# Optimization experiments

Measured on AMD Instinct MI355X. Metric: run time of the kernel, lower is better.

Reference implementation:

```python
import jax, jax.numpy as jnp
import numpy as np

PAST = 12
FUTURE = 12
INPUT_SIZE = 256
OUTPUT_SIZE = FUTURE * INPUT_SIZE  # 3072


def setup_inputs() -> dict:
    key = jax.random.key(0)
    k_inp, k_w, k_b = jax.random.split(key, 3)
    inp = jax.random.normal(k_inp, (64, 288, INPUT_SIZE), dtype=jnp.float32)
    fan_in = INPUT_SIZE * PAST
    bound = 1.0 / np.sqrt(fan_in)
    # torch nn.Linear init: U(-1/sqrt(fan_in), 1/sqrt(fan_in)); W is (out, in)
    W = jax.random.uniform(k_w, (OUTPUT_SIZE, fan_in), minval=-bound, maxval=bound, dtype=jnp.float32)
    b = jax.random.uniform(k_b, (OUTPUT_SIZE,), minval=-bound, maxval=bound, dtype=jnp.float32)
    return {"inp": inp, "W": W, "b": b}


def reference(inp, W, b):
    batch, length, dim = inp.shape
    n_win = length - PAST  # number of sliding windows (torch loop count)
    # Gather all overlapping windows at once: (batch, n_win, PAST, dim)
    idx = jnp.arange(n_win)[:, None] + jnp.arange(PAST)[None, :]
    windows = inp[:, idx, :].reshape(batch, n_win, PAST * dim)
    # One batched GEMM replaces n_win tiny Linear calls: x @ W.T + b
    out = jnp.einsum('bnk,ok->bno', windows, W) + b
    return out.reshape(batch, -1, FUTURE, dim)
```

## Files before the change

kernel.cpp:

```cpp
#include <hip/hip_runtime.h>
#include <hip/hip_bf16.h>

#define BATCH   64
#define LEN     288
#define DIM     256
#define PAST    12
#define NWIN    (LEN - PAST)
#define M_DIM   (BATCH * NWIN)
#define K_DIM   (PAST * DIM)
#define N_DIM   3072

#define BM 256
#define BN 256
#define BK 64
#define NTILE   (K_DIM / BK)
#define NITER   (NTILE / 2)
#define GRID_M  (M_DIM / BM)
#define GRID_N  (N_DIM / BN)

typedef __attribute__((ext_vector_type(8))) short bh8;
typedef __attribute__((ext_vector_type(4))) float f32x4;

__device__ __forceinline__ void llds16(const void* g, void* l) {
    __builtin_amdgcn_global_load_lds(
        (const __attribute__((address_space(1))) unsigned int*)g,
        (__attribute__((address_space(3))) unsigned int*)l,
        16, 0, 0);
}

__global__ void cvt_f32_bf16(const float* __restrict__ in,
                             __hip_bfloat16* __restrict__ out, int n8) {
    int i = blockIdx.x * blockDim.x + threadIdx.x;
    if (i >= n8) return;
    const float4* p = (const float4*)in;
    float4 a = p[2 * i], b = p[2 * i + 1];
    union { __hip_bfloat16 h[8]; int4 v; } u;
    u.h[0] = __float2bfloat16(a.x); u.h[1] = __float2bfloat16(a.y);
    u.h[2] = __float2bfloat16(a.z); u.h[3] = __float2bfloat16(a.w);
    u.h[4] = __float2bfloat16(b.x); u.h[5] = __float2bfloat16(b.y);
    u.h[6] = __float2bfloat16(b.z); u.h[7] = __float2bfloat16(b.w);
    ((int4*)out)[i] = u.v;
}


#define LDS_A(buf) (smem + (buf) * 65536)
#define LDS_B(buf) (smem + (buf) * 65536 + 32768)

#define PH_MID  __builtin_amdgcn_sched_barrier(0); __builtin_amdgcn_s_barrier(); \
                __builtin_amdgcn_sched_barrier(0); \
                asm volatile("s_waitcnt lgkmcnt(0)" ::: "memory"); \
                __builtin_amdgcn_sched_barrier(0); __builtin_amdgcn_s_setprio(1);
#define PH_END  __builtin_amdgcn_s_setprio(0); __builtin_amdgcn_sched_barrier(0); \
                __builtin_amdgcn_s_barrier(); __builtin_amdgcn_sched_barrier(0);
#define PH_END_VM __builtin_amdgcn_s_setprio(0); __builtin_amdgcn_sched_barrier(0); \
                asm volatile("s_waitcnt vmcnt(6)" ::: "memory"); \
                __builtin_amdgcn_s_barrier(); __builtin_amdgcn_sched_barrier(0);

#define RD_A4(buf, MB) { \
    const char* _b = LDS_A(buf) + aRowB; \
    _Pragma("unroll") for (int mi = 0; mi < 4; ++mi) { \
        a0[mi][0] = *(const bh8*)(_b + (MB + mi) * 2048 + kOff0); \
        a0[mi][1] = *(const bh8*)(_b + (MB + mi) * 2048 + kOff1); \
    } }
#define RD_B2(buf, dst, NB) { \
    const char* _b = LDS_B(buf) + bRowB; \
    _Pragma("unroll") for (int ni = 0; ni < 2; ++ni) { \
        dst[ni][0] = *(const bh8*)(_b + (NB + ni) * 2048 + kOff0); \
        dst[ni][1] = *(const bh8*)(_b + (NB + ni) * 2048 + kOff1); \
    } }
#define MFMA_Q(MB, NB, BB) \
    _Pragma("unroll") for (int mi = 0; mi < 4; ++mi) \
    _Pragma("unroll") for (int ni = 0; ni < 2; ++ni) { \
        acc[MB + mi][NB + ni] = __builtin_amdgcn_mfma_f32_16x16x32_bf16( \
            a0[mi][0], BB[ni][0], acc[MB + mi][NB + ni], 0, 0, 0); \
        acc[MB + mi][NB + ni] = __builtin_amdgcn_mfma_f32_16x16x32_bf16( \
            a0[mi][1], BB[ni][1], acc[MB + mi][NB + ni], 0, 0, 0); \
    }
#define STG_A1(buf, kt, q) \
    llds16(Ag + aSrc[q] + (kt) * 64, LDS_A(buf) + (q) * 8192 + wOff);
#define STG_B1(buf, kt, u) \
    llds16(Wg + bSrc[u] + (kt) * 64, LDS_B(buf) + (u) * 8192 + wOff);

__global__ __launch_bounds__(512, 2)
void gemm_win8(const __hip_bfloat16* __restrict__ Ag,
               const __hip_bfloat16* __restrict__ Wg,
               const float* __restrict__ bias,
               float* __restrict__ C)
{
    extern __shared__ char smem[];

    const int tid  = threadIdx.x;
    const int nwg = GRID_M * GRID_N;
    const int q = nwg >> 3, r = nwg & 7;
    const int xcd = blockIdx.x & 7, loc = blockIdx.x >> 3;
    const int wgid = (xcd < r ? xcd * (q + 1) : r * (q + 1) + (xcd - r) * q) + loc;
    const int bm = wgid / GRID_N;
    const int bn = wgid - bm * GRID_N;
    const int tile_m = bm * BM;
    const int tile_n = bn * BN;

    const int rd  = tid >> 3;
    const int ch  = tid & 3 ? (tid & 7) : (tid & 7);
    const int chs = (((tid & 7) ^ (rd & 7)) * 8);
    int aSrc[4], bSrc[4];
#pragma unroll
    for (int rb = 0; rb < 4; ++rb) {
        int m  = tile_m + rb * 64 + rd;
        int bq = m / NWIN;
        int wq = m - bq * NWIN;
        aSrc[rb] = (bq * LEN + wq) * DIM + chs;
        bSrc[rb] = (tile_n + rb * 64 + rd) * K_DIM + chs;
    }
    (void)ch;

    const int wave = tid >> 6, lane = tid & 63;
    const int wm = wave >> 2, wn = wave & 3;
    const int fr = lane & 15, kg = lane >> 4;
    const int sw    = (fr & 7) << 4;
    const int kOff0 = (kg * 16) ^ sw;
    const int kOff1 = kOff0 ^ 64;
    const int aRowB = (wm * 128 + fr) * 128;
    const int bRowB = (wn * 64 + fr) * 128;
    const int wOff  = wave * 1024;

    bh8 a0[4][2], fb0[2][2], fb1[2][2];
    f32x4 acc[8][4] = {};

    STG_A1(0, 0, 0); STG_A1(0, 0, 1); STG_A1(0, 0, 2); STG_A1(0, 0, 3);
    STG_B1(0, 0, 0); STG_B1(0, 0, 1); STG_B1(0, 0, 2); STG_B1(0, 0, 3);
    STG_A1(1, 1, 0); STG_A1(1, 1, 2);
    STG_B1(1, 1, 0); STG_B1(1, 1, 1);
    STG_A1(1, 1, 1); STG_A1(1, 1, 3);
    asm volatile("s_waitcnt vmcnt(6)" ::: "memory");
    __builtin_amdgcn_s_barrier();
    __builtin_amdgcn_sched_barrier(0);

#pragma unroll 1
    for (int it = 0; it < NITER; ++it) {
        const int b = 2 * it + 1;
        int c = 2 * it + 2; if (c >= NTILE) c = NTILE - 2;
        int d = 2 * it + 3; if (d >= NTILE) d = NTILE - 1;

        RD_A4(0, 0); RD_B2(0, fb0, 0);
        STG_B1(1, b, 2); STG_B1(1, b, 3);
        PH_MID; MFMA_Q(0, 0, fb0); PH_END;

        RD_B2(0, fb1, 2);
        STG_A1(0, c, 0); STG_A1(0, c, 2);
        PH_MID; MFMA_Q(0, 2, fb1); PH_END;

        RD_A4(0, 4);
        STG_B1(0, c, 0); STG_B1(0, c, 1);
        PH_MID; MFMA_Q(4, 2, fb1); PH_END;

        STG_A1(0, c, 1); STG_A1(0, c, 3);
        PH_MID; MFMA_Q(4, 0, fb0); PH_END_VM;

        RD_A4(1, 0); RD_B2(1, fb0, 0);
        STG_B1(0, c, 2); STG_B1(0, c, 3);
        PH_MID; MFMA_Q(0, 0, fb0); PH_END;

        RD_B2(1, fb1, 2);
        STG_A1(1, d, 0); STG_A1(1, d, 2);
        PH_MID; MFMA_Q(0, 2, fb1); PH_END;

        RD_A4(1, 4);
        STG_B1(1, d, 0); STG_B1(1, d, 1);
        PH_MID; MFMA_Q(4, 2, fb1); PH_END;

        STG_A1(1, d, 1); STG_A1(1, d, 3);
        PH_MID; MFMA_Q(4, 0, fb0); PH_END_VM;
    }

    float bv[4];
    const float* bp = bias + tile_n + wn * 64 + fr;
#pragma unroll
    for (int ni = 0; ni < 4; ++ni) bv[ni] = bp[ni * 16];

    const int r0 = (lane >> 4) * 4;
#pragma unroll
    for (int mi = 0; mi < 8; ++mi) {
#pragma unroll
        for (int j = 0; j < 4; ++j) {
            long m = tile_m + wm * 128 + mi * 16 + r0 + j;
            float* crow = C + m * (long)N_DIM + tile_n + wn * 64 + fr;
#pragma unroll
            for (int ni = 0; ni < 4; ++ni)
                crow[ni * 16] = acc[mi][ni][j] + bv[ni];
        }
    }
}

extern "C" void kernel_launch(void* const* d_in, const int* in_sizes, int n_in,
                              void* d_out, int out_size, void* d_ws, size_t ws_size,
                              hipStream_t stream) {
    const float* inp  = (const float*)d_in[0];
    const float* Wf   = (const float*)d_in[1];
    const float* bias = (const float*)d_in[2];
    float* out = (float*)d_out;

    __hip_bfloat16* Abf = (__hip_bfloat16*)d_ws;
    __hip_bfloat16* Wbf = (__hip_bfloat16*)((char*)d_ws + (size_t)BATCH * LEN * DIM * 2);

    const int nA8 = BATCH * LEN * DIM / 8;
    const int nW8 = N_DIM * K_DIM / 8;
    cvt_f32_bf16<<<(nA8 + 255) / 256, 256, 0, stream>>>(inp, Abf, nA8);
    cvt_f32_bf16<<<(nW8 + 255) / 256, 256, 0, stream>>>(Wf, Wbf, nW8);

    hipFuncSetAttribute((const void*)gemm_win8,
                        hipFuncAttributeMaxDynamicSharedMemorySize, 131072);
    gemm_win8<<<dim3(GRID_M * GRID_N), 512, 131072, stream>>>(Abf, Wbf, bias, out);
}
```

Measured before the change: 340.8 us.

## Split GEMM into 256x256 bulk kernel plus 128x128 tail kernel for wave quantization

M is 17664 rows, which gives 69 row-tiles of 256 and 828 workgroups, a poor fit for 256 CUs. The GEMM is now split: a bulk kernel covers the first 16384 rows with 768 workgroups of 256x256 tiles, and a separate tail kernel covers the last 1280 rows with 240 workgroups of 128x128 tiles. This is meant to reduce the partially filled last wave. Output stores also become nontemporal. The cost is an extra kernel launch and a less efficient tile shape for the tail.

After: 310.0 us. 1.1x faster.

```diff
diff --git a/kernel.cpp b/kernel.cpp
--- a/kernel.cpp
+++ b/kernel.cpp
@@ -15,8 +15,12 @@
 #define BK 64
 #define NTILE   (K_DIM / BK)
 #define NITER   (NTILE / 2)
-#define GRID_M  (M_DIM / BM)
-#define GRID_N  (N_DIM / BN)
+
+#define GRID_N   12
+#define BULK_WG  768
+#define TAIL_M0  16384
+#define TAIL_QN  24
+#define TAIL_WG  240
 
 typedef __attribute__((ext_vector_type(8))) short bh8;
 typedef __attribute__((ext_vector_type(4))) float f32x4;
@@ -42,19 +46,18 @@
     ((int4*)out)[i] = u.v;
 }
 
-
-#define LDS_A(buf) (smem + (buf) * 65536)
-#define LDS_B(buf) (smem + (buf) * 65536 + 32768)
-
 #define PH_MID  __builtin_amdgcn_sched_barrier(0); __builtin_amdgcn_s_barrier(); \
                 __builtin_amdgcn_sched_barrier(0); \
                 asm volatile("s_waitcnt lgkmcnt(0)" ::: "memory"); \
                 __builtin_amdgcn_sched_barrier(0); __builtin_amdgcn_s_setprio(1);
 #define PH_END  __builtin_amdgcn_s_setprio(0); __builtin_amdgcn_sched_barrier(0); \
                 __builtin_amdgcn_s_barrier(); __builtin_amdgcn_sched_barrier(0);
-#define PH_END_VM __builtin_amdgcn_s_setprio(0); __builtin_amdgcn_sched_barrier(0); \
-                asm volatile("s_waitcnt vmcnt(6)" ::: "memory"); \
+#define PH_END_VM(N) __builtin_amdgcn_s_setprio(0); __builtin_amdgcn_sched_barrier(0); \
+                asm volatile("s_waitcnt vmcnt(" #N ")" ::: "memory"); \
                 __builtin_amdgcn_s_barrier(); __builtin_amdgcn_sched_barrier(0);
+
+#define LDS_A(buf) (smem + (buf) * 65536)
+#define LDS_B(buf) (smem + (buf) * 65536 + 32768)
 
 #define RD_A4(buf, MB) { \
     const char* _b = LDS_A(buf) + aRowB; \
@@ -82,25 +85,21 @@
     llds16(Wg + bSrc[u] + (kt) * 64, LDS_B(buf) + (u) * 8192 + wOff);
 
 __global__ __launch_bounds__(512, 2)
-void gemm_win8(const __hip_bfloat16* __restrict__ Ag,
+void gemm_bulk(const __hip_bfloat16* __restrict__ Ag,
                const __hip_bfloat16* __restrict__ Wg,
                const float* __restrict__ bias,
                float* __restrict__ C)
 {
     extern __shared__ char smem[];
 
-    const int tid  = threadIdx.x;
-    const int nwg = GRID_M * GRID_N;
-    const int q = nwg >> 3, r = nwg & 7;
-    const int xcd = blockIdx.x & 7, loc = blockIdx.x >> 3;
-    const int wgid = (xcd < r ? xcd * (q + 1) : r * (q + 1) + (xcd - r) * q) + loc;
+    const int tid = threadIdx.x;
+    const int wgid = (blockIdx.x & 7) * (BULK_WG / 8) + (blockIdx.x >> 3);
     const int bm = wgid / GRID_N;
     const int bn = wgid - bm * GRID_N;
     const int tile_m = bm * BM;
     const int tile_n = bn * BN;
 
     const int rd  = tid >> 3;
-    const int ch  = tid & 3 ? (tid & 7) : (tid & 7);
     const int chs = (((tid & 7) ^ (rd & 7)) * 8);
     int aSrc[4], bSrc[4];
 #pragma unroll
@@ -111,7 +110,6 @@
         aSrc[rb] = (bq * LEN + wq) * DIM + chs;
         bSrc[rb] = (tile_n + rb * 64 + rd) * K_DIM + chs;
     }
-    (void)ch;
 
     const int wave = tid >> 6, lane = tid & 63;
     const int wm = wave >> 2, wn = wave & 3;
@@ -154,7 +152,7 @@
         PH_MID; MFMA_Q(4, 2, fb1); PH_END;
 
         STG_A1(0, c, 1); STG_A1(0, c, 3);
-        PH_MID; MFMA_Q(4, 0, fb0); PH_END_VM;
+        PH_MID; MFMA_Q(4, 0, fb0); PH_END_VM(6);
 
         RD_A4(1, 0); RD_B2(1, fb0, 0);
         STG_B1(0, c, 2); STG_B1(0, c, 3);
@@ -169,7 +167,7 @@
         PH_MID; MFMA_Q(4, 2, fb1); PH_END;
 
         STG_A1(1, d, 1); STG_A1(1, d, 3);
-        PH_MID; MFMA_Q(4, 0, fb0); PH_END_VM;
+        PH_MID; MFMA_Q(4, 0, fb0); PH_END_VM(6);
     }
 
     float bv[4];
@@ -186,7 +184,120 @@
             float* crow = C + m * (long)N_DIM + tile_n + wn * 64 + fr;
 #pragma unroll
             for (int ni = 0; ni < 4; ++ni)
-                crow[ni * 16] = acc[mi][ni][j] + bv[ni];
+                __builtin_nontemporal_store(acc[mi][ni][j] + bv[ni], &crow[ni * 16]);
+        }
+    }
+}
+
+#define TLDS_A(buf) (smem + (buf) * 32768)
+#define TLDS_B(buf) (smem + (buf) * 32768 + 16384)
+
+#define T_RD(buf) { \
+    const char* _a = TLDS_A(buf) + aRowB; \
+    _Pragma("unroll") for (int mi = 0; mi < 4; ++mi) { \
+        a0[mi][0] = *(const bh8*)(_a + mi * 2048 + kOff0); \
+        a0[mi][1] = *(const bh8*)(_a + mi * 2048 + kOff1); \
+    } \
+    const char* _bb = TLDS_B(buf) + bRowB; \
+    _Pragma("unroll") for (int ni = 0; ni < 2; ++ni) { \
+        fb0[ni][0] = *(const bh8*)(_bb + ni * 2048 + kOff0); \
+        fb0[ni][1] = *(const bh8*)(_bb + ni * 2048 + kOff1); \
+    } }
+#define T_MFMA(MB) \
+    _Pragma("unroll") for (int mi = 0; mi < 2; ++mi) \
+    _Pragma("unroll") for (int ni = 0; ni < 2; ++ni) { \
+        acc[MB + mi][ni] = __builtin_amdgcn_mfma_f32_16x16x32_bf16( \
+            a0[MB + mi][0], fb0[ni][0], acc[MB + mi][ni], 0, 0, 0); \
+        acc[MB + mi][ni] = __builtin_amdgcn_mfma_f32_16x16x32_bf16( \
+            a0[MB + mi][1], fb0[ni][1], acc[MB + mi][ni], 0, 0, 0); \
+    }
+#define T_STG_A(buf, kt, u) \
+    llds16(Ag + aSrc[u] + (kt) * 64, TLDS_A(buf) + (u) * 8192 + wOff);
+#define T_STG_B(buf, kt, u) \
+    llds16(Wg + bSrc[u] + (kt) * 64, TLDS_B(buf) + (u) * 8192 + wOff);
+
+__global__ __launch_bounds__(512, 2)
+void gemm_tail(const __hip_bfloat16* __restrict__ Ag,
+               const __hip_bfloat16* __restrict__ Wg,
+               const float* __restrict__ bias,
+               float* __restrict__ C)
+{
+    extern __shared__ char smem[];
+
+    const int tid = threadIdx.x;
+    const int wgid = (blockIdx.x & 7) * (TAIL_WG / 8) + (blockIdx.x >> 3);
+    const int qm = wgid / TAIL_QN;
+    const int qn = wgid - qm * TAIL_QN;
+    const int tile_m = TAIL_M0 + qm * 128;
+    const int tile_n = qn * 128;
+
+    const int rd  = tid >> 3;
+    const int chs = (((tid & 7) ^ (rd & 7)) * 8);
+    int aSrc[2], bSrc[2];
+#pragma unroll
+    for (int rb = 0; rb < 2; ++rb) {
+        int m  = tile_m + rb * 64 + rd;
+        int bq = m / NWIN;
+        int wq = m - bq * NWIN;
+        aSrc[rb] = (bq * LEN + wq) * DIM + chs;
+        bSrc[rb] = (tile_n + rb * 64 + rd) * K_DIM + chs;
+    }
+
+    const int wave = tid >> 6, lane = tid & 63;
+    const int wm = wave >> 2, wn = wave & 3;
+    const int fr = lane & 15, kg = lane >> 4;
+    const int sw    = (fr & 7) << 4;
+    const int kOff0 = (kg * 16) ^ sw;
+    const int kOff1 = kOff0 ^ 64;
+    const int aRowB = (wm * 64 + fr) * 128;
+    const int bRowB = (wn * 32 + fr) * 128;
+    const int wOff  = wave * 1024;
+
+    bh8 a0[4][2], fb0[2][2];
+    f32x4 acc[4][2] = {};
+
+    T_STG_A(0, 0, 0); T_STG_A(0, 0, 1); T_STG_B(0, 0, 0); T_STG_B(0, 0, 1);
+    T_STG_A(1, 1, 0); T_STG_A(1, 1, 1);
+    asm volatile("s_waitcnt vmcnt(2)" ::: "memory");
+    __builtin_amdgcn_s_barrier();
+    __builtin_amdgcn_sched_barrier(0);
+
+#pragma unroll 1
+    for (int it = 0; it < NITER; ++it) {
+        const int b = 2 * it + 1;
+        int c = 2 * it + 2; if (c >= NTILE) c = NTILE - 2;
+        int d = 2 * it + 3; if (d >= NTILE) d = NTILE - 1;
+
+        T_RD(0);
+        T_STG_B(1, b, 0); T_STG_B(1, b, 1);
+        PH_MID; T_MFMA(0); PH_END;
+
+        T_STG_A(0, c, 0); T_STG_A(0, c, 1);
+        PH_MID; T_MFMA(2); PH_END_VM(2);
+
+        T_RD(1);
+        T_STG_B(0, c, 0); T_STG_B(0, c, 1);
+        PH_MID; T_MFMA(0); PH_END;
+
+        T_STG_A(1, d, 0); T_STG_A(1, d, 1);
+        PH_MID; T_MFMA(2); PH_END_VM(2);
+    }
+
+    float bv[2];
+    const float* bp = bias + tile_n + wn * 32 + fr;
+#pragma unroll
+    for (int ni = 0; ni < 2; ++ni) bv[ni] = bp[ni * 16];
+
+    const int r0 = (lane >> 4) * 4;
+#pragma unroll
+    for (int mi = 0; mi < 4; ++mi) {
+#pragma unroll
+        for (int j = 0; j < 4; ++j) {
+            long m = tile_m + wm * 64 + mi * 16 + r0 + j;
+            float* crow = C + m * (long)N_DIM + tile_n + wn * 32 + fr;
+#pragma unroll
+            for (int ni = 0; ni < 2; ++ni)
+                __builtin_nontemporal_store(acc[mi][ni][j] + bv[ni], &crow[ni * 16]);
         }
     }
 }
@@ -207,7 +318,10 @@
     cvt_f32_bf16<<<(nA8 + 255) / 256, 256, 0, stream>>>(inp, Abf, nA8);
     cvt_f32_bf16<<<(nW8 + 255) / 256, 256, 0, stream>>>(Wf, Wbf, nW8);
 
-    hipFuncSetAttribute((const void*)gemm_win8,
+    hipFuncSetAttribute((const void*)gemm_bulk,
                         hipFuncAttributeMaxDynamicSharedMemorySize, 131072);
-    gemm_win8<<<dim3(GRID_M * GRID_N), 512, 131072, stream>>>(Abf, Wbf, bias, out);
-}
+    hipFuncSetAttribute((const void*)gemm_tail,
+                        hipFuncAttributeMaxDynamicSharedMemorySize, 65536);
+    gemm_bulk<<<dim3(BULK_WG), 512, 131072, stream>>>(Abf, Wbf, bias, out);
+    gemm_tail<<<dim3(TAIL_WG), 512, 65536, stream>>>(Abf, Wbf, bias, out);
+}
```
